# Performance work log

Measured on AMD Instinct MI355X. Metric: run time of the kernel, lower is better.

## Reference

```python
import jax, jax.numpy as jnp
import numpy as np

B, C, H, W = 8, 192, 128, 128
NH = 4  # num_heads
EPS = 1e-12


def setup_inputs() -> dict:
    key = jax.random.key(0)
    ks = jax.random.split(key, 10)
    s = 1.0 / np.sqrt(C)
    return {
        "x_q": jax.random.normal(ks[0], (B, C, H, W), jnp.float32),
        "x_k": jax.random.normal(ks[1], (B, C, H, W), jnp.float32),
        "Wq": jax.random.uniform(ks[2], (C, C), jnp.float32, -s, s),
        "bq": jax.random.uniform(ks[3], (C,), jnp.float32, -s, s),
        "Wkv": jax.random.uniform(ks[4], (2 * C, C), jnp.float32, -s, s),
        "bkv": jax.random.uniform(ks[5], (2 * C,), jnp.float32, -s, s),
        "Wp": jax.random.uniform(ks[6], (C, C), jnp.float32, -s, s),
        "bp": jax.random.uniform(ks[7], (C,), jnp.float32, -s, s),
        "temperature": jnp.ones((NH, 1, 1), jnp.float32),
    }


def _l2norm(x, axis):
    # torch F.normalize: x / clamp_min(||x||, eps)
    n = jnp.sqrt(jnp.sum(x * x, axis=axis, keepdims=True))
    return x / jnp.maximum(n, EPS)


def reference(x_q, x_k, Wq, bq, Wkv, bkv, Wp, bp, temperature):
    # 1x1 convs == channel matmuls
    q = jnp.einsum('oc,bchw->bohw', Wq, x_q) + bq[:, None, None]
    kv = jnp.einsum('oc,bchw->bohw', Wkv, x_k) + bkv[:, None, None]
    k, v = jnp.split(kv, 2, axis=1)

    def heads(t):  # (B,C,H,W) -> (B,NH,C//NH, H*W)
        return t.reshape(B, NH, C // NH, H * W)

    q, k, v = heads(q), heads(k), heads(v)
    q = _l2norm(q, 2)
    k = _l2norm(k, 2)

    attn_scale = 0.1 * jax.nn.sigmoid(temperature)  # (NH,1,1)
    attn = jnp.einsum('bhcd,bhkd->bhck', q, k) * attn_scale
    attn = jax.nn.softmax(attn, axis=-1)
    out = jnp.einsum('bhck,bhkd->bhcd', attn, v)
    out = out.reshape(B, C, H, W)
    out = jnp.einsum('oc,bchw->bohw', Wp, out) + bp[:, None, None]
    return out
```

## Files before the change

### kernel.cpp

```cpp
#include <hip/hip_runtime.h>
#include <hip/hip_bf16.h>

#define HW 16384
#define CC 192
#define BB 8
#define NHD 4
#define HD 48

typedef __attribute__((ext_vector_type(8))) short  short8;
typedef __attribute__((ext_vector_type(4))) float  f32x4;

static __device__ __forceinline__ unsigned short f2bf(float f) {
  unsigned u = __float_as_uint(f);
  u += 0x7fffu + ((u >> 16) & 1u);
  return (unsigned short)(u >> 16);
}
static __device__ __forceinline__ unsigned pk2bf(float lo, float hi) {
  __hip_bfloat162 h = __float22bfloat162_rn(make_float2(lo, hi));
  return *reinterpret_cast<unsigned*>(&h);
}

static __device__ __forceinline__ void ldsbar() {
  asm volatile("" ::: "memory");
  asm volatile("s_waitcnt lgkmcnt(0)" ::: "memory");
  __builtin_amdgcn_s_barrier();
  asm volatile("" ::: "memory");
}

#define SWZ_COL(row, cdw) ((cdw) ^ ((((row) >> 3) & 3) << 2))

__global__ __launch_bounds__(256) void cast_w_kernel(
    const float* __restrict__ Wq, const float* __restrict__ Wkv,
    unsigned short* __restrict__ Wb)
{
  const int i = blockIdx.x * 256 + threadIdx.x;
  const float v = (i < CC*CC) ? Wq[i] : Wkv[i - CC*CC];
  Wb[i] = f2bf(v);
}

__global__ __launch_bounds__(256, 2) void qkg_kernel(
    const float* __restrict__ x_q, const float* __restrict__ x_k,
    const unsigned short* __restrict__ wb,
    const float* __restrict__ bq, const float* __restrict__ bkv,
    float* __restrict__ gpart)
{
  const int tid  = threadIdx.x;
  const int lane = tid & 63;
  const int wv   = tid >> 6;
  const int b    = blockIdx.y;
  const int p0   = blockIdx.x * 256;
  const int l15  = lane & 15;
  const int lg   = lane >> 4;
  const int qd   = tid & 15;

  __shared__ unsigned short Xs[64][200];
  __shared__ unsigned short QN[NHD][48][68];
  __shared__ unsigned short KN[NHD][48][68];

  const float* Xq = x_q + (size_t)b*CC*HW;
  const float* Xk = x_k + (size_t)b*CC*HW;

  f32x4 pre[12];
  auto LOADT = [&](const float* X, int pb) {
    #pragma unroll
    for (int i = 0; i < 6; ++i) {
      const int cp = (tid >> 4) + i*16;
      const float* base = X + (size_t)(2*cp)*HW + pb + qd*4;
      pre[2*i]   = *(const f32x4*)(base);
      pre[2*i+1] = *(const f32x4*)(base + HW);
    }
  };
  auto WRITET = [&]() {
    #pragma unroll
    for (int i = 0; i < 6; ++i) {
      const int cp = (tid >> 4) + i*16;
      #pragma unroll
      for (int j = 0; j < 4; ++j) {
        const int row = qd*4 + j;
        *(unsigned*)&Xs[row][2*SWZ_COL(row, cp)] =
            pk2bf(pre[2*i][j], pre[2*i+1][j]);
      }
    }
  };

  auto PROJ = [&](const unsigned short* W, const float* bias,
                  unsigned short (*DST)[68]) {
    f32x4 acc[3][4];
    #pragma unroll
    for (int mt = 0; mt < 3; ++mt)
      #pragma unroll
      for (int nt = 0; nt < 4; ++nt)
        acc[mt][nt] = (f32x4){0.f, 0.f, 0.f, 0.f};

    #pragma unroll
    for (int kk = 0; kk < 6; ++kk) {
      short8 afr[3], bfr[4];
      #pragma unroll
      for (int mt = 0; mt < 3; ++mt)
        afr[mt] = *(const short8*)(W + (size_t)(wv*48 + mt*16 + l15)*CC + kk*32 + lg*8);
      #pragma unroll
      for (int nt = 0; nt < 4; ++nt) {
        const int lgs = lg ^ ((2*nt + (l15 >> 3)) & 3);
        bfr[nt] = *(const short8*)&Xs[nt*16 + l15][kk*32 + lgs*8];
      }
      #pragma unroll
      for (int mt = 0; mt < 3; ++mt)
        #pragma unroll
        for (int nt = 0; nt < 4; ++nt)
          acc[mt][nt] = __builtin_amdgcn_mfma_f32_16x16x32_bf16(
              afr[mt], bfr[nt], acc[mt][nt], 0, 0, 0);
    }

    #pragma unroll
    for (int nt = 0; nt < 4; ++nt) {
      float v[3][4];
      float ss = 0.f;
      #pragma unroll
      for (int mt = 0; mt < 3; ++mt)
        #pragma unroll
        for (int r = 0; r < 4; ++r) {
          const float x = acc[mt][nt][r] + bias[wv*48 + mt*16 + lg*4 + r];
          v[mt][r] = x;
          ss += x*x;
        }
      ss += __shfl_xor(ss, 16);
      ss += __shfl_xor(ss, 32);
      const float rn = 1.0f / fmaxf(sqrtf(ss), 1e-12f);
      #pragma unroll
      for (int mt = 0; mt < 3; ++mt)
        #pragma unroll
        for (int r = 0; r < 4; ++r)
          DST[mt*16 + lg*4 + r][nt*16 + l15] = f2bf(v[mt][r] * rn);
    }
  };

  f32x4 gacc[3][3];
  #pragma unroll
  for (int mt = 0; mt < 3; ++mt)
    #pragma unroll
    for (int nt = 0; nt < 3; ++nt)
      gacc[mt][nt] = (f32x4){0.f, 0.f, 0.f, 0.f};

  LOADT(Xq, p0);
  for (int t = 0; t < 4; ++t) {
    const int pb = p0 + t*64;
    WRITET();
    ldsbar();
    LOADT(Xk, pb);
    PROJ(wb, bq, QN[wv]);
    ldsbar();
    WRITET();
    ldsbar();
    if (t < 3) LOADT(Xq, pb + 64);
    PROJ(wb + (size_t)CC*CC, bkv, KN[wv]);
    ldsbar();

    #pragma unroll
    for (int s = 0; s < 2; ++s) {
      short8 ga[3], gb[3];
      #pragma unroll
      for (int mt = 0; mt < 3; ++mt)
        ga[mt] = *(const short8*)&QN[wv][mt*16 + l15][s*32 + lg*8];
      #pragma unroll
      for (int nt = 0; nt < 3; ++nt)
        gb[nt] = *(const short8*)&KN[wv][nt*16 + l15][s*32 + lg*8];
      #pragma unroll
      for (int mt = 0; mt < 3; ++mt)
        #pragma unroll
        for (int nt = 0; nt < 3; ++nt)
          gacc[mt][nt] = __builtin_amdgcn_mfma_f32_16x16x32_bf16(
              ga[mt], gb[nt], gacc[mt][nt], 0, 0, 0);
    }
  }

  float* G = gpart + ((size_t)(b*NHD + wv)*64 + blockIdx.x)*2304;
  #pragma unroll
  for (int mt = 0; mt < 3; ++mt)
    #pragma unroll
    for (int nt = 0; nt < 3; ++nt)
      #pragma unroll
      for (int r = 0; r < 4; ++r)
        G[(mt*16 + lg*4 + r)*HD + nt*16 + l15] = gacc[mt][nt][r];
}

__global__ __launch_bounds__(256) void proj_fin(
    const float* __restrict__ x_k,
    const unsigned short* __restrict__ w3b,
    const float* __restrict__ b3,
    float* __restrict__ of)
{
  const int tid  = threadIdx.x;
  const int lane = tid & 63;
  const int wv   = tid >> 6;
  const int b    = blockIdx.y;
  const int p0   = blockIdx.x * 256;
  const int l15  = lane & 15;
  const int lg   = lane >> 4;
  const int qd   = tid & 15;

  __shared__ unsigned short Xt[2][64][200];

  const float* X = x_k + (size_t)b*CC*HW;
  const unsigned short* Wb = w3b + (size_t)b*CC*CC;
  const float* bias = b3 + (size_t)b*CC;

  short8 afr[6][3];
  #pragma unroll
  for (int kk = 0; kk < 6; ++kk)
    #pragma unroll
    for (int mt = 0; mt < 3; ++mt)
      afr[kk][mt] = *(const short8*)(Wb + (size_t)(wv*48 + mt*16 + l15)*CC + kk*32 + lg*8);

  float bv[3][4];
  #pragma unroll
  for (int mt = 0; mt < 3; ++mt)
    #pragma unroll
    for (int r = 0; r < 4; ++r)
      bv[mt][r] = bias[wv*48 + mt*16 + lg*4 + r];

  f32x4 pre[12];
  auto LOADT = [&](int pb) {
    #pragma unroll
    for (int i = 0; i < 6; ++i) {
      const int cp = (tid >> 4) + i*16;
      const float* base = X + (size_t)(2*cp)*HW + pb + qd*4;
      pre[2*i]   = *(const f32x4*)(base);
      pre[2*i+1] = *(const f32x4*)(base + HW);
    }
  };
  auto WRITET = [&](int buf) {
    #pragma unroll
    for (int i = 0; i < 6; ++i) {
      const int cp = (tid >> 4) + i*16;
      #pragma unroll
      for (int j = 0; j < 4; ++j) {
        const int row = qd*4 + j;
        *(unsigned*)&Xt[buf][row][2*SWZ_COL(row, cp)] =
            pk2bf(pre[2*i][j], pre[2*i+1][j]);
      }
    }
  };

  float* Ofp = of + (size_t)b*CC*HW;

  auto COMPUTE = [&](int buf, int pb) {
    f32x4 acc[3][4];
    #pragma unroll
    for (int mt = 0; mt < 3; ++mt)
      #pragma unroll
      for (int nt = 0; nt < 4; ++nt)
        acc[mt][nt] = (f32x4){0.f, 0.f, 0.f, 0.f};

    #pragma unroll
    for (int kk = 0; kk < 6; ++kk) {
      short8 bfr[4];
      #pragma unroll
      for (int nt = 0; nt < 4; ++nt) {
        const int lgs = lg ^ ((2*nt + (l15 >> 3)) & 3);
        bfr[nt] = *(const short8*)&Xt[buf][nt*16 + l15][kk*32 + lgs*8];
      }
      #pragma unroll
      for (int mt = 0; mt < 3; ++mt)
        #pragma unroll
        for (int nt = 0; nt < 4; ++nt)
          acc[mt][nt] = __builtin_amdgcn_mfma_f32_16x16x32_bf16(
              afr[kk][mt], bfr[nt], acc[mt][nt], 0, 0, 0);
    }

    #pragma unroll
    for (int nt = 0; nt < 4; ++nt) {
      const int col = pb + nt*16 + l15;
      #pragma unroll
      for (int mt = 0; mt < 3; ++mt)
        #pragma unroll
        for (int r = 0; r < 4; ++r)
          Ofp[(size_t)(wv*48 + mt*16 + lg*4 + r)*HW + col] = acc[mt][nt][r] + bv[mt][r];
    }
  };

  LOADT(p0);
  WRITET(0);
  ldsbar();
  #pragma unroll
  for (int t = 0; t < 4; ++t) {
    if (t < 3) LOADT(p0 + (t+1)*64);
    COMPUTE(t & 1, p0 + t*64);
    if (t < 3) {
      WRITET((t & 1) ^ 1);
      ldsbar();
    }
  }
}

__global__ __launch_bounds__(256) void attn_m_kernel(
    const float* __restrict__ Gpart,
    const float* __restrict__ Wp,
    const float* __restrict__ temp,
    float* __restrict__ Mf)
{
  __shared__ float att[HD][52];
  const int bh  = blockIdx.x;
  const int b   = bh >> 2, h = bh & 3;
  const int tid = threadIdx.x;
  const float* src = Gpart + (size_t)bh*64*2304;

  #pragma unroll
  for (int i = 0; i < 9; ++i) {
    const int e = tid + i*256;
    float s = 0.f;
    #pragma unroll
    for (int k = 0; k < 64; ++k) s += src[(size_t)k*2304 + e];
    att[e/48][e%48] = s;
  }
  __syncthreads();

  const int g = tid >> 2, sl = tid & 3;
  if (g < HD) {
    const float t = temp[h];
    const float scale = 0.1f / (1.0f + expf(-t));
    float* row = att[g];
    float m = -1e30f;
    #pragma unroll
    for (int jj = 0; jj < 12; ++jj) m = fmaxf(m, row[sl + jj*4]);
    m = fmaxf(m, __shfl_xor(m, 1));
    m = fmaxf(m, __shfl_xor(m, 2));
    float ev[12];
    float s = 0.f;
    #pragma unroll
    for (int jj = 0; jj < 12; ++jj) {
      const float e = expf((row[sl + jj*4] - m) * scale);
      ev[jj] = e; s += e;
    }
    s += __shfl_xor(s, 1);
    s += __shfl_xor(s, 2);
    const float inv = 1.0f / s;
    #pragma unroll
    for (int jj = 0; jj < 12; ++jj) row[sl + jj*4] = ev[jj] * inv;
  }
  __syncthreads();

  #pragma unroll
  for (int i = 0; i < 36; ++i) {
    const int idx = tid + i*256;
    const int o = idx / HD, k2 = idx % HD;
    const float* wrow = Wp + (size_t)o*CC + h*HD;
    float s = 0.f;
    #pragma unroll
    for (int c = 0; c < HD; ++c) s += wrow[c] * att[c][k2];
    Mf[(size_t)b*CC*CC + (size_t)o*CC + h*HD + k2] = s;
  }
}

__global__ __launch_bounds__(192) void w3_kernel(
    const float* __restrict__ Mf, const float* __restrict__ Wkv,
    const float* __restrict__ bkv, const float* __restrict__ bp,
    unsigned short* __restrict__ W3b, float* __restrict__ b3)
{
  const int b  = blockIdx.x;
  const int o0 = blockIdx.y * 8;
  const int j  = threadIdx.x;
  const float* M  = Mf + ((size_t)b*CC + o0)*CC;
  const float* Wv = Wkv + (size_t)CC*CC;
  const float* bv = bkv + CC;

  float acc[8]  = {0.f,0.f,0.f,0.f,0.f,0.f,0.f,0.f};
  float bacc[8] = {0.f,0.f,0.f,0.f,0.f,0.f,0.f,0.f};
  #pragma unroll 4
  for (int k = 0; k < CC; ++k) {
    const float w  = Wv[(size_t)k*CC + j];
    const float bk = bv[k];
    #pragma unroll
    for (int r = 0; r < 8; ++r) {
      const float m = M[r*CC + k];
      acc[r]  += m * w;
      bacc[r] += m * bk;
    }
  }
  unsigned short* dst = W3b + ((size_t)b*CC + o0)*CC + j;
  #pragma unroll
  for (int r = 0; r < 8; ++r) dst[(size_t)r*CC] = f2bf(acc[r]);
  if (j < 8) b3[(size_t)b*CC + o0 + j] = bacc[j] + bp[o0 + j];
}

extern "C" void kernel_launch(void* const* d_in, const int* in_sizes, int n_in,
                              void* d_out, int out_size, void* d_ws, size_t ws_size,
                              hipStream_t stream)
{
  (void)in_sizes; (void)n_in; (void)out_size; (void)ws_size;
  const float* x_q  = (const float*)d_in[0];
  const float* x_k  = (const float*)d_in[1];
  const float* Wq   = (const float*)d_in[2];
  const float* bq   = (const float*)d_in[3];
  const float* Wkv  = (const float*)d_in[4];
  const float* bkv  = (const float*)d_in[5];
  const float* Wp   = (const float*)d_in[6];
  const float* bp   = (const float*)d_in[7];
  const float* temp = (const float*)d_in[8];

  char* p = (char*)d_ws;
  float* gpart = (float*)p;                 p += (size_t)BB*NHD*64*2304*sizeof(float);
  float* mf = (float*)p;                    p += (size_t)BB*CC*CC*sizeof(float);
  unsigned short* w3b = (unsigned short*)p; p += (size_t)BB*CC*CC*sizeof(unsigned short);
  float* b3 = (float*)p;                    p += (size_t)BB*CC*sizeof(float);
  unsigned short* wb = (unsigned short*)p;

  cast_w_kernel<<<dim3((2*CC*CC)/256), 256, 0, stream>>>(Wq, Wkv, wb);

  qkg_kernel<<<dim3(HW/256, BB), 256, 0, stream>>>(
      x_q, x_k, wb, bq, bkv, gpart);

  attn_m_kernel<<<dim3(BB*NHD), 256, 0, stream>>>(gpart, Wp, temp, mf);
  w3_kernel<<<dim3(BB, 24), 192, 0, stream>>>(mf, Wkv, bkv, bp, w3b, b3);

  proj_fin<<<dim3(HW/256, BB), 256, 0, stream>>>(x_k, w3b, b3, (float*)d_out);
}
```

Baseline: 167.8 us.

## Split qkg kernel into Q and K wave-halves with register-resident weights

The qkg kernel now uses 512-thread blocks. The first four waves project Q and the other four project K at the same time, each into its own LDS staging buffer, where before one set of waves did Q and K one after the other. Each wave keeps its bf16 weight fragments and biases in registers for the whole kernel instead of reloading them from global memory every tile. Each half also accumulates a different half of the Gram inner dimension, and the partial results go to separate gpart slots. The intent is fewer serialized barriers and less repeated weight traffic, at the cost of more registers per thread (afr alone is 18 short8 values) and a possible occupancy drop.

```diff
diff --git a/kernel.cpp b/kernel.cpp
--- a/kernel.cpp
+++ b/kernel.cpp
@@ -38,7 +38,7 @@
   Wb[i] = f2bf(v);
 }
 
-__global__ __launch_bounds__(256, 2) void qkg_kernel(
+__global__ __launch_bounds__(512, 2) void qkg_kernel(
     const float* __restrict__ x_q, const float* __restrict__ x_k,
     const unsigned short* __restrict__ wb,
     const float* __restrict__ bq, const float* __restrict__ bkv,
@@ -47,25 +47,46 @@
   const int tid  = threadIdx.x;
   const int lane = tid & 63;
   const int wv   = tid >> 6;
+  const int half = wv >> 2;
+  const int hh   = wv & 3;
   const int b    = blockIdx.y;
-  const int p0   = blockIdx.x * 256;
+  const int p0   = blockIdx.x * 512;
   const int l15  = lane & 15;
   const int lg   = lane >> 4;
-  const int qd   = tid & 15;
-
-  __shared__ unsigned short Xs[64][200];
+  const int ht   = tid & 255;
+  const int qd   = ht & 15;
+
+  __shared__ unsigned short Xsq[64][200];
+  __shared__ unsigned short Xsk[64][200];
   __shared__ unsigned short QN[NHD][48][68];
   __shared__ unsigned short KN[NHD][48][68];
 
-  const float* Xq = x_q + (size_t)b*CC*HW;
-  const float* Xk = x_k + (size_t)b*CC*HW;
+  const float* Xsrc = (half ? x_k : x_q) + (size_t)b*CC*HW;
+  unsigned short (*Xdst)[200] = half ? Xsk : Xsq;
+  unsigned short (*DST)[68]   = half ? KN[hh] : QN[hh];
+
+  const unsigned short* W = wb + (size_t)half*CC*CC;
+  short8 afr[6][3];
+  #pragma unroll
+  for (int kk = 0; kk < 6; ++kk)
+    #pragma unroll
+    for (int mt = 0; mt < 3; ++mt)
+      afr[kk][mt] = *(const short8*)(W + (size_t)(hh*48 + mt*16 + l15)*CC + kk*32 + lg*8);
+
+  const float* bias = half ? bkv : bq;
+  float bv[3][4];
+  #pragma unroll
+  for (int mt = 0; mt < 3; ++mt)
+    #pragma unroll
+    for (int r = 0; r < 4; ++r)
+      bv[mt][r] = bias[hh*48 + mt*16 + lg*4 + r];
 
   f32x4 pre[12];
-  auto LOADT = [&](const float* X, int pb) {
+  auto LOADT = [&](int pb) {
     #pragma unroll
     for (int i = 0; i < 6; ++i) {
-      const int cp = (tid >> 4) + i*16;
-      const float* base = X + (size_t)(2*cp)*HW + pb + qd*4;
+      const int cp = (ht >> 4) + i*16;
+      const float* base = Xsrc + (size_t)(2*cp)*HW + pb + qd*4;
       pre[2*i]   = *(const f32x4*)(base);
       pre[2*i+1] = *(const f32x4*)(base + HW);
     }
@@ -73,18 +94,29 @@
   auto WRITET = [&]() {
     #pragma unroll
     for (int i = 0; i < 6; ++i) {
-      const int cp = (tid >> 4) + i*16;
+      const int cp = (ht >> 4) + i*16;
       #pragma unroll
       for (int j = 0; j < 4; ++j) {
         const int row = qd*4 + j;
-        *(unsigned*)&Xs[row][2*SWZ_COL(row, cp)] =
+        *(unsigned*)&Xdst[row][2*SWZ_COL(row, cp)] =
             pk2bf(pre[2*i][j], pre[2*i+1][j]);
       }
     }
   };
 
-  auto PROJ = [&](const unsigned short* W, const float* bias,
-                  unsigned short (*DST)[68]) {
+  f32x4 gacc[3][3];
+  #pragma unroll
+  for (int mt = 0; mt < 3; ++mt)
+    #pragma unroll
+    for (int nt = 0; nt < 3; ++nt)
+      gacc[mt][nt] = (f32x4){0.f, 0.f, 0.f, 0.f};
+
+  LOADT(p0);
+  for (int t = 0; t < 8; ++t) {
+    WRITET();
+    ldsbar();
+    if (t < 7) LOADT(p0 + (t+1)*64);
+
     f32x4 acc[3][4];
     #pragma unroll
     for (int mt = 0; mt < 3; ++mt)
@@ -94,21 +126,18 @@
 
     #pragma unroll
     for (int kk = 0; kk < 6; ++kk) {
-      short8 afr[3], bfr[4];
-      #pragma unroll
-      for (int mt = 0; mt < 3; ++mt)
-        afr[mt] = *(const short8*)(W + (size_t)(wv*48 + mt*16 + l15)*CC + kk*32 + lg*8);
+      short8 bfr[4];
       #pragma unroll
       for (int nt = 0; nt < 4; ++nt) {
         const int lgs = lg ^ ((2*nt + (l15 >> 3)) & 3);
-        bfr[nt] = *(const short8*)&Xs[nt*16 + l15][kk*32 + lgs*8];
+        bfr[nt] = *(const short8*)&Xdst[nt*16 + l15][kk*32 + lgs*8];
       }
       #pragma unroll
       for (int mt = 0; mt < 3; ++mt)
         #pragma unroll
         for (int nt = 0; nt < 4; ++nt)
           acc[mt][nt] = __builtin_amdgcn_mfma_f32_16x16x32_bf16(
-              afr[mt], bfr[nt], acc[mt][nt], 0, 0, 0);
+              afr[kk][mt], bfr[nt], acc[mt][nt], 0, 0, 0);
     }
 
     #pragma unroll
@@ -119,7 +148,7 @@
       for (int mt = 0; mt < 3; ++mt)
         #pragma unroll
         for (int r = 0; r < 4; ++r) {
-          const float x = acc[mt][nt][r] + bias[wv*48 + mt*16 + lg*4 + r];
+          const float x = acc[mt][nt][r] + bv[mt][r];
           v[mt][r] = x;
           ss += x*x;
         }
@@ -132,38 +161,17 @@
         for (int r = 0; r < 4; ++r)
           DST[mt*16 + lg*4 + r][nt*16 + l15] = f2bf(v[mt][r] * rn);
     }
-  };
-
-  f32x4 gacc[3][3];
-  #pragma unroll
-  for (int mt = 0; mt < 3; ++mt)
-    #pragma unroll
-    for (int nt = 0; nt < 3; ++nt)
-      gacc[mt][nt] = (f32x4){0.f, 0.f, 0.f, 0.f};
-
-  LOADT(Xq, p0);
-  for (int t = 0; t < 4; ++t) {
-    const int pb = p0 + t*64;
-    WRITET();
     ldsbar();
-    LOADT(Xk, pb);
-    PROJ(wb, bq, QN[wv]);
-    ldsbar();
-    WRITET();
-    ldsbar();
-    if (t < 3) LOADT(Xq, pb + 64);
-    PROJ(wb + (size_t)CC*CC, bkv, KN[wv]);
-    ldsbar();
-
-    #pragma unroll
-    for (int s = 0; s < 2; ++s) {
+
+    {
+      const int s = half;
       short8 ga[3], gb[3];
       #pragma unroll
       for (int mt = 0; mt < 3; ++mt)
-        ga[mt] = *(const short8*)&QN[wv][mt*16 + l15][s*32 + lg*8];
+        ga[mt] = *(const short8*)&QN[hh][mt*16 + l15][s*32 + lg*8];
       #pragma unroll
       for (int nt = 0; nt < 3; ++nt)
-        gb[nt] = *(const short8*)&KN[wv][nt*16 + l15][s*32 + lg*8];
+        gb[nt] = *(const short8*)&KN[hh][nt*16 + l15][s*32 + lg*8];
       #pragma unroll
       for (int mt = 0; mt < 3; ++mt)
         #pragma unroll
@@ -173,7 +181,7 @@
     }
   }
 
-  float* G = gpart + ((size_t)(b*NHD + wv)*64 + blockIdx.x)*2304;
+  float* G = gpart + ((size_t)(b*NHD + hh)*64 + blockIdx.x*2 + half)*2304;
   #pragma unroll
   for (int mt = 0; mt < 3; ++mt)
     #pragma unroll
@@ -406,7 +414,7 @@
 
   cast_w_kernel<<<dim3((2*CC*CC)/256), 256, 0, stream>>>(Wq, Wkv, wb);
 
-  qkg_kernel<<<dim3(HW/256, BB), 256, 0, stream>>>(
+  qkg_kernel<<<dim3(HW/512, BB), 512, 0, stream>>>(
       x_q, x_k, wb, bq, bkv, gpart);
 
   attn_m_kernel<<<dim3(BB*NHD), 256, 0, stream>>>(gpart, Wp, temp, mf);
```

Result: slower. 173.2 us (+3.2%).
